# Kernel tuning notes

Hardware: AMD Instinct MI355X
Metric: run time of the kernel (lower is better)

The kernel has to match this reference:

```python
import jax, jax.numpy as jnp
import numpy as np

N_NODES = 50000
N_EDGES = 800000
IN_DIM = 128
OUT_DIM = 64


def setup_inputs() -> dict:
    key = jax.random.key(0)
    k1, k2, k3, k4 = jax.random.split(key, 4)
    x = jax.random.normal(k1, (N_NODES, IN_DIM), dtype=jnp.float32)
    edge_index = jax.random.randint(k2, (2, N_EDGES), 0, N_NODES, dtype=jnp.int64)
    # learned params: W: Linear(in_dim, out_dim, bias=False); att: Linear(2*out_dim, 1, bias=False)
    W = jax.random.normal(k3, (IN_DIM, OUT_DIM), dtype=jnp.float32) * 0.05
    att = jax.random.normal(k4, (2 * OUT_DIM, 1), dtype=jnp.float32) * 0.05
    return {"x": x, "edge_index": edge_index, "W": W, "att": att}


def reference(x, edge_index, W, att):
    n = x.shape[0]
    h = x @ W  # [N, D]
    src, dst = edge_index[0], edge_index[1]
    # per-edge attention logit: leaky_relu(att^T [h_src ; h_dst])
    e = jnp.concatenate([h[src], h[dst]], axis=-1) @ att  # [E, 1]
    e = jax.nn.leaky_relu(e[:, 0], negative_slope=0.2)  # [E]
    # segment softmax over edges grouped by destination node
    m = jax.ops.segment_max(e, dst, num_segments=n)  # [N]
    ex = jnp.exp(e - m[dst])  # [E]
    denom = jax.ops.segment_sum(ex, dst, num_segments=n)  # [N]
    alpha = ex / denom[dst]  # [E]
    # weighted scatter-add aggregation
    agg = jax.ops.segment_sum(alpha[:, None] * h[src], dst, num_segments=n)  # [N, D]
    return jax.nn.elu(agg)
```

## Files before the change

### kernel.cpp

```cpp
#include <hip/hip_runtime.h>
#include <hip/hip_bf16.h>
#include <hip/hip_fp16.h>
#include <math.h>

#define N_NODES 50000
#define N_EDGES 800000
#define IN_DIM 128
#define OUT_DIM 64

typedef __attribute__((ext_vector_type(8))) short bf16x8;
typedef __attribute__((ext_vector_type(4))) float f32x4;

static __device__ __forceinline__ ushort f2bf(float f) {
  uint u = __float_as_uint(f);
  uint r = (u + 0x7fffu + ((u >> 16) & 1u)) >> 16;
  return (ushort)r;
}
static __device__ __forceinline__ float bf2f(ushort h) {
  return __uint_as_float(((uint)h) << 16);
}

__global__ __launch_bounds__(256) void k1_mfma(
    const float* __restrict__ x, const float* __restrict__ W,
    const float* __restrict__ att,
    __half* __restrict__ h, float* __restrict__ a1, float* __restrict__ a2,
    int* __restrict__ deg) {
  __shared__ __align__(16) ushort Ah[64 * 128];
  __shared__ __align__(16) ushort Al[64 * 128];
  __shared__ __align__(16) ushort Bh[64 * 128];
  __shared__ __align__(16) ushort Bl[64 * 128];

  int tid = threadIdx.x;
  int row0 = blockIdx.x * 64;

  if (tid < 64) {
    int g = row0 + tid;
    if (g < N_NODES) deg[g] = 0;
  }

#pragma unroll
  for (int it = 0; it < 8; ++it) {
    int i4 = it * 256 + tid;
    int row = i4 >> 5;
    int kq = i4 & 31;
    int grow = row0 + row;
    if (grow > N_NODES - 1) grow = N_NODES - 1;
    float4 v = ((const float4*)x)[(size_t)grow * 32 + kq];
    ushort4 hi, lo;
    hi.x = f2bf(v.x); lo.x = f2bf(v.x - bf2f(hi.x));
    hi.y = f2bf(v.y); lo.y = f2bf(v.y - bf2f(hi.y));
    hi.z = f2bf(v.z); lo.z = f2bf(v.z - bf2f(hi.z));
    hi.w = f2bf(v.w); lo.w = f2bf(v.w - bf2f(hi.w));
    int idx = (row * 128 + kq * 4) ^ ((row & 7) << 3);
    *(ushort4*)&Ah[idx] = hi;
    *(ushort4*)&Al[idx] = lo;
  }

  {
    int c = tid & 63, kq = tid >> 6;
#pragma unroll
    for (int jj = 0; jj < 4; ++jj) {
      int kb = kq * 32 + jj * 8;
      uint4 ph, pl;
      uint hp[8], lp[8];
#pragma unroll
      for (int q = 0; q < 8; ++q) {
        float wv = W[(size_t)(kb + q) * OUT_DIM + c];
        ushort hh = f2bf(wv);
        hp[q] = hh;
        lp[q] = f2bf(wv - bf2f(hh));
      }
      ph.x = hp[0] | (hp[1] << 16); ph.y = hp[2] | (hp[3] << 16);
      ph.z = hp[4] | (hp[5] << 16); ph.w = hp[6] | (hp[7] << 16);
      pl.x = lp[0] | (lp[1] << 16); pl.y = lp[2] | (lp[3] << 16);
      pl.z = lp[4] | (lp[5] << 16); pl.w = lp[6] | (lp[7] << 16);
      int idx = (c * 128 + kb) ^ ((c & 7) << 3);
      *(uint4*)&Bh[idx] = ph;
      *(uint4*)&Bl[idx] = pl;
    }
  }
  __syncthreads();

  int w = tid >> 6, l = tid & 63;
  int ml = l & 15, kg = l >> 4;

  f32x4 acc[4];
#pragma unroll
  for (int nt = 0; nt < 4; ++nt) acc[nt] = (f32x4){0.f, 0.f, 0.f, 0.f};

#pragma unroll
  for (int ks = 0; ks < 4; ++ks) {
    int arow = w * 16 + ml;
    int aidx = (arow * 128 + ks * 32 + kg * 8) ^ ((arow & 7) << 3);
    bf16x8 a_h = *(const bf16x8*)&Ah[aidx];
    bf16x8 a_l = *(const bf16x8*)&Al[aidx];
#pragma unroll
    for (int nt = 0; nt < 4; ++nt) {
      int brow = nt * 16 + ml;
      int bidx = (brow * 128 + ks * 32 + kg * 8) ^ ((brow & 7) << 3);
      bf16x8 b_h = *(const bf16x8*)&Bh[bidx];
      bf16x8 b_l = *(const bf16x8*)&Bl[bidx];
      acc[nt] = __builtin_amdgcn_mfma_f32_16x16x32_bf16(a_h, b_h, acc[nt], 0, 0, 0);
      acc[nt] = __builtin_amdgcn_mfma_f32_16x16x32_bf16(a_l, b_h, acc[nt], 0, 0, 0);
      acc[nt] = __builtin_amdgcn_mfma_f32_16x16x32_bf16(a_h, b_l, acc[nt], 0, 0, 0);
    }
  }

  float t1[4], t2[4];
#pragma unroll
  for (int nt = 0; nt < 4; ++nt) {
    t1[nt] = att[nt * 16 + ml];
    t2[nt] = att[OUT_DIM + nt * 16 + ml];
  }
#pragma unroll
  for (int r = 0; r < 4; ++r) {
    int drow = kg * 4 + r;
    int grow = row0 + w * 16 + drow;
    bool ok = grow < N_NODES;
    float p1 = 0.f, p2 = 0.f;
#pragma unroll
    for (int nt = 0; nt < 4; ++nt) {
      float d = acc[nt][r];
      if (ok) h[(size_t)grow * OUT_DIM + nt * 16 + ml] = __float2half(d);
      p1 = fmaf(d, t1[nt], p1);
      p2 = fmaf(d, t2[nt], p2);
    }
#pragma unroll
    for (int o = 1; o <= 8; o <<= 1) {
      p1 += __shfl_xor(p1, o, 64);
      p2 += __shfl_xor(p2, o, 64);
    }
    if (ml == 0 && ok) { a1[grow] = p1; a2[grow] = p2; }
  }
}

#define K2_T (N_EDGES / 8)
__global__ __launch_bounds__(256) void k2_rank(const int* __restrict__ dstp,
                                               int* __restrict__ deg,
                                               int* __restrict__ rank) {
  int t = blockIdx.x * 256 + threadIdx.x;
  if (t >= K2_T) return;
  int4 d0 = ((const int4*)dstp)[t * 2];
  int4 d1 = ((const int4*)dstp)[t * 2 + 1];
  int4 r0, r1;
  r0.x = atomicAdd(&deg[d0.x], 1);
  r0.y = atomicAdd(&deg[d0.y], 1);
  r0.z = atomicAdd(&deg[d0.z], 1);
  r0.w = atomicAdd(&deg[d0.w], 1);
  r1.x = atomicAdd(&deg[d1.x], 1);
  r1.y = atomicAdd(&deg[d1.y], 1);
  r1.z = atomicAdd(&deg[d1.z], 1);
  r1.w = atomicAdd(&deg[d1.w], 1);
  ((int4*)rank)[t * 2] = r0;
  ((int4*)rank)[t * 2 + 1] = r1;
}

#define N4 (N_NODES / 4)
#define SCAN_NB ((N4 + 255) / 256)

__global__ __launch_bounds__(256) void k3a_scan(const int* __restrict__ deg,
                                                int* __restrict__ off,
                                                int* __restrict__ bsum) {
  __shared__ int sw[4];
  int tid = threadIdx.x, lane = tid & 63, wid = tid >> 6;
  int i4 = blockIdx.x * 256 + tid;
  int4 v = make_int4(0, 0, 0, 0);
  if (i4 < N4) v = ((const int4*)deg)[i4];
  int local = v.x + v.y + v.z + v.w;
  int incl = local;
#pragma unroll
  for (int o = 1; o < 64; o <<= 1) {
    int t = __shfl_up(incl, o, 64);
    if (lane >= o) incl += t;
  }
  if (lane == 63) sw[wid] = incl;
  __syncthreads();
  if (tid == 0) {
    int c = 0;
#pragma unroll
    for (int ww = 0; ww < 4; ++ww) { int t = sw[ww]; sw[ww] = c; c += t; }
    bsum[blockIdx.x] = c;
  }
  __syncthreads();
  int excl = incl - local + sw[wid];
  int4 o;
  o.x = excl; o.y = o.x + v.x; o.z = o.y + v.y; o.w = o.z + v.z;
  if (i4 < N4) ((int4*)off)[i4] = o;
}

__global__ __launch_bounds__(256) void k3c_add(int* __restrict__ off,
                                               const int* __restrict__ bsum,
                                               const float* __restrict__ a2,
                                               int2* __restrict__ oa2) {
  __shared__ int sb[64];
  int tid = threadIdx.x;
  if (tid < 64) {
    int v = (tid < SCAN_NB) ? bsum[tid] : 0;
    int incl = v;
#pragma unroll
    for (int o = 1; o < 64; o <<= 1) {
      int t = __shfl_up(incl, o, 64);
      if (tid >= o) incl += t;
    }
    sb[tid] = incl - v;
  }
  __syncthreads();
  int i4 = blockIdx.x * 256 + tid;
  if (i4 == 0) off[N_NODES] = N_EDGES;
  if (i4 >= N4) return;
  int add = sb[blockIdx.x];
  int4 v = ((const int4*)off)[i4];
  v.x += add; v.y += add; v.z += add; v.w += add;
  ((int4*)off)[i4] = v;
  float4 a = ((const float4*)a2)[i4];
  int4 p0 = make_int4(v.x, __float_as_int(a.x), v.y, __float_as_int(a.y));
  int4 p1 = make_int4(v.z, __float_as_int(a.z), v.w, __float_as_int(a.w));
  ((int4*)oa2)[i4 * 2] = p0;
  ((int4*)oa2)[i4 * 2 + 1] = p1;
}

#define K4_T (N_EDGES / 4)
__global__ __launch_bounds__(256) void k4_scatter(
    const int* __restrict__ src, const int* __restrict__ dstp,
    const int* __restrict__ rank,
    const float* __restrict__ a1, const int2* __restrict__ oa2,
    int2* __restrict__ sedge) {
  int t = blockIdx.x * 256 + threadIdx.x;
  if (t >= K4_T) return;
  int4 s = ((const int4*)src)[t];
  int4 d = ((const int4*)dstp)[t];
  int4 r = ((const int4*)rank)[t];
  float A0 = a1[s.x], A1 = a1[s.y], A2 = a1[s.z], A3 = a1[s.w];
  int2 O0 = oa2[d.x], O1 = oa2[d.y], O2 = oa2[d.z], O3 = oa2[d.w];
  float e0 = A0 + __int_as_float(O0.y);
  float e1 = A1 + __int_as_float(O1.y);
  float e2 = A2 + __int_as_float(O2.y);
  float e3 = A3 + __int_as_float(O3.y);
  e0 = e0 > 0.f ? e0 : 0.2f * e0;
  e1 = e1 > 0.f ? e1 : 0.2f * e1;
  e2 = e2 > 0.f ? e2 : 0.2f * e2;
  e3 = e3 > 0.f ? e3 : 0.2f * e3;
  sedge[O0.x + r.x] = make_int2(s.x, __float_as_int(__expf(e0)));
  sedge[O1.x + r.y] = make_int2(s.y, __float_as_int(__expf(e1)));
  sedge[O2.x + r.z] = make_int2(s.z, __float_as_int(__expf(e2)));
  sedge[O3.x + r.w] = make_int2(s.w, __float_as_int(__expf(e3)));
}

__global__ __launch_bounds__(256) void k5_agg(
    const int* __restrict__ off, const int2* __restrict__ sedge,
    const __half* __restrict__ h, float* __restrict__ out) {
  int tid = threadIdx.x;
  int g = tid >> 4, gl = tid & 15;
  int n = blockIdx.x * 16 + g;
  if (n >= N_NODES) return;
  int b = off[n], e = off[n + 1];

  float sum = 0.f;
  float acc0 = 0.f, acc1 = 0.f, acc2 = 0.f, acc3 = 0.f;
  const __half* __restrict__ hb = h;

  int j = b;
  for (; j + 3 < e; j += 4) {
    int2 s0 = sedge[j], s1 = sedge[j + 1], s2 = sedge[j + 2], s3 = sedge[j + 3];
    uint2 r0 = *(const uint2*)(hb + (size_t)s0.x * OUT_DIM + 4 * gl);
    uint2 r1 = *(const uint2*)(hb + (size_t)s1.x * OUT_DIM + 4 * gl);
    uint2 r2 = *(const uint2*)(hb + (size_t)s2.x * OUT_DIM + 4 * gl);
    uint2 r3 = *(const uint2*)(hb + (size_t)s3.x * OUT_DIM + 4 * gl);
    float w0 = __int_as_float(s0.y), w1 = __int_as_float(s1.y);
    float w2 = __int_as_float(s2.y), w3 = __int_as_float(s3.y);
    sum += (w0 + w1) + (w2 + w3);
    float2 f;
    f = __half22float2(__builtin_bit_cast(__half2, r0.x)); acc0 = fmaf(w0, f.x, acc0); acc1 = fmaf(w0, f.y, acc1);
    f = __half22float2(__builtin_bit_cast(__half2, r0.y)); acc2 = fmaf(w0, f.x, acc2); acc3 = fmaf(w0, f.y, acc3);
    f = __half22float2(__builtin_bit_cast(__half2, r1.x)); acc0 = fmaf(w1, f.x, acc0); acc1 = fmaf(w1, f.y, acc1);
    f = __half22float2(__builtin_bit_cast(__half2, r1.y)); acc2 = fmaf(w1, f.x, acc2); acc3 = fmaf(w1, f.y, acc3);
    f = __half22float2(__builtin_bit_cast(__half2, r2.x)); acc0 = fmaf(w2, f.x, acc0); acc1 = fmaf(w2, f.y, acc1);
    f = __half22float2(__builtin_bit_cast(__half2, r2.y)); acc2 = fmaf(w2, f.x, acc2); acc3 = fmaf(w2, f.y, acc3);
    f = __half22float2(__builtin_bit_cast(__half2, r3.x)); acc0 = fmaf(w3, f.x, acc0); acc1 = fmaf(w3, f.y, acc1);
    f = __half22float2(__builtin_bit_cast(__half2, r3.y)); acc2 = fmaf(w3, f.x, acc2); acc3 = fmaf(w3, f.y, acc3);
  }
  for (; j < e; ++j) {
    int2 s0 = sedge[j];
    uint2 r0 = *(const uint2*)(hb + (size_t)s0.x * OUT_DIM + 4 * gl);
    float w0 = __int_as_float(s0.y);
    sum += w0;
    float2 f;
    f = __half22float2(__builtin_bit_cast(__half2, r0.x)); acc0 = fmaf(w0, f.x, acc0); acc1 = fmaf(w0, f.y, acc1);
    f = __half22float2(__builtin_bit_cast(__half2, r0.y)); acc2 = fmaf(w0, f.x, acc2); acc3 = fmaf(w0, f.y, acc3);
  }

  float inv = (e > b) ? 1.f / sum : 0.f;
  acc0 *= inv; acc1 *= inv; acc2 *= inv; acc3 *= inv;
  float4 o4;
  o4.x = acc0 > 0.f ? acc0 : (__expf(acc0) - 1.f);
  o4.y = acc1 > 0.f ? acc1 : (__expf(acc1) - 1.f);
  o4.z = acc2 > 0.f ? acc2 : (__expf(acc2) - 1.f);
  o4.w = acc3 > 0.f ? acc3 : (__expf(acc3) - 1.f);
  ((float4*)(out + (size_t)n * OUT_DIM))[gl] = o4;
}

extern "C" void kernel_launch(void* const* d_in, const int* in_sizes, int n_in,
                              void* d_out, int out_size, void* d_ws, size_t ws_size,
                              hipStream_t stream) {
  const float* x   = (const float*)d_in[0];
  const int*   ei  = (const int*)d_in[1];
  const float* W   = (const float*)d_in[2];
  const float* att = (const float*)d_in[3];
  float* out = (float*)d_out;

  char* p = (char*)d_ws;
  __half* h  = (__half*)p;  p += (size_t)N_NODES * OUT_DIM * sizeof(__half);
  float* a1  = (float*)p;   p += (size_t)N_NODES * sizeof(float);
  float* a2  = (float*)p;   p += (size_t)N_NODES * sizeof(float);
  int*   deg = (int*)p;     p += (size_t)N_NODES * sizeof(int);
  int*   off = (int*)p;     p += (size_t)(N_NODES + 4) * sizeof(int);
  int2*  oa2 = (int2*)p;    p += (size_t)N_NODES * sizeof(int2);
  int*   rank = (int*)p;    p += (size_t)N_EDGES * sizeof(int);
  int2*  sedge = (int2*)p;  p += (size_t)N_EDGES * sizeof(int2);
  int*   bsum = (int*)p;    p += 64 * sizeof(int);

  const int* src  = ei;
  const int* dstp = ei + N_EDGES;

  k1_mfma<<<(N_NODES + 63) / 64, 256, 0, stream>>>(x, W, att, h, a1, a2, deg);
  k2_rank<<<(K2_T + 255) / 256, 256, 0, stream>>>(dstp, deg, rank);
  k3a_scan<<<SCAN_NB, 256, 0, stream>>>(deg, off, bsum);
  k3c_add<<<SCAN_NB, 256, 0, stream>>>(off, bsum, a2, oa2);
  k4_scatter<<<(K4_T + 255) / 256, 256, 0, stream>>>(src, dstp, rank, a1, oa2, sedge);
  k5_agg<<<(N_NODES + 15) / 16, 256, 0, stream>>>(off, sedge, h, out);
}
```

Baseline: 97.54 us.

## Fuse rank counting into GEMM launch, drop W low-part MFMA, widen gathers

Splits the degree-zeroing into its own small kernel and merges the edge-rank atomic pass with the projection GEMM into one launch, with separate block ranges for each, so the two independent phases can overlap. The GEMM drops the bf16 low-part of W and its third MFMA per tile, which lowers the precision of h. The scatter kernel now handles 8 edges per thread. The aggregation kernel uses 8 lanes per node with 16-byte loads of h rows instead of 16 lanes with 8-byte loads.

```diff
diff --git a/kernel.cpp b/kernel.cpp
--- a/kernel.cpp
+++ b/kernel.cpp
@@ -20,23 +20,49 @@
   return __uint_as_float(((uint)h) << 16);
 }
 
-__global__ __launch_bounds__(256) void k1_mfma(
+#define N4 (N_NODES / 4)
+#define SCAN_NB ((N4 + 255) / 256)
+#define RANK_NB ((N_EDGES / 8 + 255) / 256)
+#define GEMM_NB ((N_NODES + 63) / 64)
+#define K2_T (N_EDGES / 8)
+#define K4_T (N_EDGES / 8)
+
+__global__ __launch_bounds__(256) void k0_zero(int* __restrict__ deg) {
+  int i4 = blockIdx.x * 256 + threadIdx.x;
+  if (i4 < N4) ((int4*)deg)[i4] = make_int4(0, 0, 0, 0);
+}
+
+__global__ __launch_bounds__(256) void k12_fused(
     const float* __restrict__ x, const float* __restrict__ W,
-    const float* __restrict__ att,
+    const float* __restrict__ att, const int* __restrict__ dstp,
     __half* __restrict__ h, float* __restrict__ a1, float* __restrict__ a2,
-    int* __restrict__ deg) {
+    int* __restrict__ deg, int* __restrict__ rank) {
   __shared__ __align__(16) ushort Ah[64 * 128];
   __shared__ __align__(16) ushort Al[64 * 128];
   __shared__ __align__(16) ushort Bh[64 * 128];
-  __shared__ __align__(16) ushort Bl[64 * 128];
 
   int tid = threadIdx.x;
-  int row0 = blockIdx.x * 64;
-
-  if (tid < 64) {
-    int g = row0 + tid;
-    if (g < N_NODES) deg[g] = 0;
-  }
+
+  if (blockIdx.x < RANK_NB) {
+    int t = blockIdx.x * 256 + tid;
+    if (t >= K2_T) return;
+    int4 d0 = ((const int4*)dstp)[t * 2];
+    int4 d1 = ((const int4*)dstp)[t * 2 + 1];
+    int4 r0, r1;
+    r0.x = atomicAdd(&deg[d0.x], 1);
+    r0.y = atomicAdd(&deg[d0.y], 1);
+    r0.z = atomicAdd(&deg[d0.z], 1);
+    r0.w = atomicAdd(&deg[d0.w], 1);
+    r1.x = atomicAdd(&deg[d1.x], 1);
+    r1.y = atomicAdd(&deg[d1.y], 1);
+    r1.z = atomicAdd(&deg[d1.z], 1);
+    r1.w = atomicAdd(&deg[d1.w], 1);
+    ((int4*)rank)[t * 2] = r0;
+    ((int4*)rank)[t * 2 + 1] = r1;
+    return;
+  }
+
+  int row0 = (blockIdx.x - RANK_NB) * 64;
 
 #pragma unroll
   for (int it = 0; it < 8; ++it) {
@@ -61,22 +87,14 @@
 #pragma unroll
     for (int jj = 0; jj < 4; ++jj) {
       int kb = kq * 32 + jj * 8;
-      uint4 ph, pl;
-      uint hp[8], lp[8];
-#pragma unroll
-      for (int q = 0; q < 8; ++q) {
-        float wv = W[(size_t)(kb + q) * OUT_DIM + c];
-        ushort hh = f2bf(wv);
-        hp[q] = hh;
-        lp[q] = f2bf(wv - bf2f(hh));
-      }
+      uint4 ph;
+      uint hp[8];
+#pragma unroll
+      for (int q = 0; q < 8; ++q) hp[q] = f2bf(W[(size_t)(kb + q) * OUT_DIM + c]);
       ph.x = hp[0] | (hp[1] << 16); ph.y = hp[2] | (hp[3] << 16);
       ph.z = hp[4] | (hp[5] << 16); ph.w = hp[6] | (hp[7] << 16);
-      pl.x = lp[0] | (lp[1] << 16); pl.y = lp[2] | (lp[3] << 16);
-      pl.z = lp[4] | (lp[5] << 16); pl.w = lp[6] | (lp[7] << 16);
       int idx = (c * 128 + kb) ^ ((c & 7) << 3);
       *(uint4*)&Bh[idx] = ph;
-      *(uint4*)&Bl[idx] = pl;
     }
   }
   __syncthreads();
@@ -99,10 +117,8 @@
       int brow = nt * 16 + ml;
       int bidx = (brow * 128 + ks * 32 + kg * 8) ^ ((brow & 7) << 3);
       bf16x8 b_h = *(const bf16x8*)&Bh[bidx];
-      bf16x8 b_l = *(const bf16x8*)&Bl[bidx];
       acc[nt] = __builtin_amdgcn_mfma_f32_16x16x32_bf16(a_h, b_h, acc[nt], 0, 0, 0);
       acc[nt] = __builtin_amdgcn_mfma_f32_16x16x32_bf16(a_l, b_h, acc[nt], 0, 0, 0);
-      acc[nt] = __builtin_amdgcn_mfma_f32_16x16x32_bf16(a_h, b_l, acc[nt], 0, 0, 0);
     }
   }
 
@@ -133,30 +149,6 @@
     if (ml == 0 && ok) { a1[grow] = p1; a2[grow] = p2; }
   }
 }
-
-#define K2_T (N_EDGES / 8)
-__global__ __launch_bounds__(256) void k2_rank(const int* __restrict__ dstp,
-                                               int* __restrict__ deg,
-                                               int* __restrict__ rank) {
-  int t = blockIdx.x * 256 + threadIdx.x;
-  if (t >= K2_T) return;
-  int4 d0 = ((const int4*)dstp)[t * 2];
-  int4 d1 = ((const int4*)dstp)[t * 2 + 1];
-  int4 r0, r1;
-  r0.x = atomicAdd(&deg[d0.x], 1);
-  r0.y = atomicAdd(&deg[d0.y], 1);
-  r0.z = atomicAdd(&deg[d0.z], 1);
-  r0.w = atomicAdd(&deg[d0.w], 1);
-  r1.x = atomicAdd(&deg[d1.x], 1);
-  r1.y = atomicAdd(&deg[d1.y], 1);
-  r1.z = atomicAdd(&deg[d1.z], 1);
-  r1.w = atomicAdd(&deg[d1.w], 1);
-  ((int4*)rank)[t * 2] = r0;
-  ((int4*)rank)[t * 2 + 1] = r1;
-}
-
-#define N4 (N_NODES / 4)
-#define SCAN_NB ((N4 + 255) / 256)
 
 __global__ __launch_bounds__(256) void k3a_scan(const int* __restrict__ deg,
                                                 int* __restrict__ off,
@@ -219,7 +211,6 @@
   ((int4*)oa2)[i4 * 2 + 1] = p1;
 }
 
-#define K4_T (N_EDGES / 4)
 __global__ __launch_bounds__(256) void k4_scatter(
     const int* __restrict__ src, const int* __restrict__ dstp,
     const int* __restrict__ rank,
@@ -227,76 +218,87 @@
     int2* __restrict__ sedge) {
   int t = blockIdx.x * 256 + threadIdx.x;
   if (t >= K4_T) return;
-  int4 s = ((const int4*)src)[t];
-  int4 d = ((const int4*)dstp)[t];
-  int4 r = ((const int4*)rank)[t];
-  float A0 = a1[s.x], A1 = a1[s.y], A2 = a1[s.z], A3 = a1[s.w];
-  int2 O0 = oa2[d.x], O1 = oa2[d.y], O2 = oa2[d.z], O3 = oa2[d.w];
-  float e0 = A0 + __int_as_float(O0.y);
-  float e1 = A1 + __int_as_float(O1.y);
-  float e2 = A2 + __int_as_float(O2.y);
-  float e3 = A3 + __int_as_float(O3.y);
-  e0 = e0 > 0.f ? e0 : 0.2f * e0;
-  e1 = e1 > 0.f ? e1 : 0.2f * e1;
-  e2 = e2 > 0.f ? e2 : 0.2f * e2;
-  e3 = e3 > 0.f ? e3 : 0.2f * e3;
-  sedge[O0.x + r.x] = make_int2(s.x, __float_as_int(__expf(e0)));
-  sedge[O1.x + r.y] = make_int2(s.y, __float_as_int(__expf(e1)));
-  sedge[O2.x + r.z] = make_int2(s.z, __float_as_int(__expf(e2)));
-  sedge[O3.x + r.w] = make_int2(s.w, __float_as_int(__expf(e3)));
+  int4 s0 = ((const int4*)src)[t * 2],  s1 = ((const int4*)src)[t * 2 + 1];
+  int4 d0 = ((const int4*)dstp)[t * 2], d1 = ((const int4*)dstp)[t * 2 + 1];
+  int4 r0 = ((const int4*)rank)[t * 2], r1 = ((const int4*)rank)[t * 2 + 1];
+  float A[8];
+  A[0] = a1[s0.x]; A[1] = a1[s0.y]; A[2] = a1[s0.z]; A[3] = a1[s0.w];
+  A[4] = a1[s1.x]; A[5] = a1[s1.y]; A[6] = a1[s1.z]; A[7] = a1[s1.w];
+  int2 O[8];
+  O[0] = oa2[d0.x]; O[1] = oa2[d0.y]; O[2] = oa2[d0.z]; O[3] = oa2[d0.w];
+  O[4] = oa2[d1.x]; O[5] = oa2[d1.y]; O[6] = oa2[d1.z]; O[7] = oa2[d1.w];
+  int S[8] = {s0.x, s0.y, s0.z, s0.w, s1.x, s1.y, s1.z, s1.w};
+  int R[8] = {r0.x, r0.y, r0.z, r0.w, r1.x, r1.y, r1.z, r1.w};
+#pragma unroll
+  for (int q = 0; q < 8; ++q) {
+    float e = A[q] + __int_as_float(O[q].y);
+    e = e > 0.f ? e : 0.2f * e;
+    sedge[O[q].x + R[q]] = make_int2(S[q], __float_as_int(__expf(e)));
+  }
 }
 
 __global__ __launch_bounds__(256) void k5_agg(
     const int* __restrict__ off, const int2* __restrict__ sedge,
     const __half* __restrict__ h, float* __restrict__ out) {
   int tid = threadIdx.x;
-  int g = tid >> 4, gl = tid & 15;
-  int n = blockIdx.x * 16 + g;
+  int g = tid >> 3, gl = tid & 7;
+  int n = blockIdx.x * 32 + g;
   if (n >= N_NODES) return;
   int b = off[n], e = off[n + 1];
 
   float sum = 0.f;
-  float acc0 = 0.f, acc1 = 0.f, acc2 = 0.f, acc3 = 0.f;
+  float a0 = 0.f, a1_ = 0.f, a2_ = 0.f, a3 = 0.f;
+  float a4 = 0.f, a5 = 0.f, a6 = 0.f, a7 = 0.f;
   const __half* __restrict__ hb = h;
+
+#define K5_ACC(rr, ww)                                                        \
+  {                                                                           \
+    float2 f;                                                                 \
+    f = __half22float2(__builtin_bit_cast(__half2, rr.x));                    \
+    a0 = fmaf(ww, f.x, a0); a1_ = fmaf(ww, f.y, a1_);                         \
+    f = __half22float2(__builtin_bit_cast(__half2, rr.y));                    \
+    a2_ = fmaf(ww, f.x, a2_); a3 = fmaf(ww, f.y, a3);                         \
+    f = __half22float2(__builtin_bit_cast(__half2, rr.z));                    \
+    a4 = fmaf(ww, f.x, a4); a5 = fmaf(ww, f.y, a5);                           \
+    f = __half22float2(__builtin_bit_cast(__half2, rr.w));                    \
+    a6 = fmaf(ww, f.x, a6); a7 = fmaf(ww, f.y, a7);                           \
+  }
 
   int j = b;
   for (; j + 3 < e; j += 4) {
     int2 s0 = sedge[j], s1 = sedge[j + 1], s2 = sedge[j + 2], s3 = sedge[j + 3];
-    uint2 r0 = *(const uint2*)(hb + (size_t)s0.x * OUT_DIM + 4 * gl);
-    uint2 r1 = *(const uint2*)(hb + (size_t)s1.x * OUT_DIM + 4 * gl);
-    uint2 r2 = *(const uint2*)(hb + (size_t)s2.x * OUT_DIM + 4 * gl);
-    uint2 r3 = *(const uint2*)(hb + (size_t)s3.x * OUT_DIM + 4 * gl);
+    uint4 r0 = ((const uint4*)(hb + (size_t)s0.x * OUT_DIM))[gl];
+    uint4 r1 = ((const uint4*)(hb + (size_t)s1.x * OUT_DIM))[gl];
+    uint4 r2 = ((const uint4*)(hb + (size_t)s2.x * OUT_DIM))[gl];
+    uint4 r3 = ((const uint4*)(hb + (size_t)s3.x * OUT_DIM))[gl];
     float w0 = __int_as_float(s0.y), w1 = __int_as_float(s1.y);
     float w2 = __int_as_float(s2.y), w3 = __int_as_float(s3.y);
     sum += (w0 + w1) + (w2 + w3);
-    float2 f;
-    f = __half22float2(__builtin_bit_cast(__half2, r0.x)); acc0 = fmaf(w0, f.x, acc0); acc1 = fmaf(w0, f.y, acc1);
-    f = __half22float2(__builtin_bit_cast(__half2, r0.y)); acc2 = fmaf(w0, f.x, acc2); acc3 = fmaf(w0, f.y, acc3);
-    f = __half22float2(__builtin_bit_cast(__half2, r1.x)); acc0 = fmaf(w1, f.x, acc0); acc1 = fmaf(w1, f.y, acc1);
-    f = __half22float2(__builtin_bit_cast(__half2, r1.y)); acc2 = fmaf(w1, f.x, acc2); acc3 = fmaf(w1, f.y, acc3);
-    f = __half22float2(__builtin_bit_cast(__half2, r2.x)); acc0 = fmaf(w2, f.x, acc0); acc1 = fmaf(w2, f.y, acc1);
-    f = __half22float2(__builtin_bit_cast(__half2, r2.y)); acc2 = fmaf(w2, f.x, acc2); acc3 = fmaf(w2, f.y, acc3);
-    f = __half22float2(__builtin_bit_cast(__half2, r3.x)); acc0 = fmaf(w3, f.x, acc0); acc1 = fmaf(w3, f.y, acc1);
-    f = __half22float2(__builtin_bit_cast(__half2, r3.y)); acc2 = fmaf(w3, f.x, acc2); acc3 = fmaf(w3, f.y, acc3);
+    K5_ACC(r0, w0); K5_ACC(r1, w1); K5_ACC(r2, w2); K5_ACC(r3, w3);
   }
   for (; j < e; ++j) {
     int2 s0 = sedge[j];
-    uint2 r0 = *(const uint2*)(hb + (size_t)s0.x * OUT_DIM + 4 * gl);
+    uint4 r0 = ((const uint4*)(hb + (size_t)s0.x * OUT_DIM))[gl];
     float w0 = __int_as_float(s0.y);
     sum += w0;
-    float2 f;
-    f = __half22float2(__builtin_bit_cast(__half2, r0.x)); acc0 = fmaf(w0, f.x, acc0); acc1 = fmaf(w0, f.y, acc1);
-    f = __half22float2(__builtin_bit_cast(__half2, r0.y)); acc2 = fmaf(w0, f.x, acc2); acc3 = fmaf(w0, f.y, acc3);
+    K5_ACC(r0, w0);
   }
 
   float inv = (e > b) ? 1.f / sum : 0.f;
-  acc0 *= inv; acc1 *= inv; acc2 *= inv; acc3 *= inv;
-  float4 o4;
-  o4.x = acc0 > 0.f ? acc0 : (__expf(acc0) - 1.f);
-  o4.y = acc1 > 0.f ? acc1 : (__expf(acc1) - 1.f);
-  o4.z = acc2 > 0.f ? acc2 : (__expf(acc2) - 1.f);
-  o4.w = acc3 > 0.f ? acc3 : (__expf(acc3) - 1.f);
-  ((float4*)(out + (size_t)n * OUT_DIM))[gl] = o4;
+  a0 *= inv; a1_ *= inv; a2_ *= inv; a3 *= inv;
+  a4 *= inv; a5 *= inv; a6 *= inv; a7 *= inv;
+  float4 o0, o1;
+  o0.x = a0 > 0.f ? a0 : (__expf(a0) - 1.f);
+  o0.y = a1_ > 0.f ? a1_ : (__expf(a1_) - 1.f);
+  o0.z = a2_ > 0.f ? a2_ : (__expf(a2_) - 1.f);
+  o0.w = a3 > 0.f ? a3 : (__expf(a3) - 1.f);
+  o1.x = a4 > 0.f ? a4 : (__expf(a4) - 1.f);
+  o1.y = a5 > 0.f ? a5 : (__expf(a5) - 1.f);
+  o1.z = a6 > 0.f ? a6 : (__expf(a6) - 1.f);
+  o1.w = a7 > 0.f ? a7 : (__expf(a7) - 1.f);
+  float4* ob = (float4*)(out + (size_t)n * OUT_DIM);
+  ob[gl * 2] = o0;
+  ob[gl * 2 + 1] = o1;
 }
 
 extern "C" void kernel_launch(void* const* d_in, const int* in_sizes, int n_in,
@@ -322,10 +324,10 @@
   const int* src  = ei;
   const int* dstp = ei + N_EDGES;
 
-  k1_mfma<<<(N_NODES + 63) / 64, 256, 0, stream>>>(x, W, att, h, a1, a2, deg);
-  k2_rank<<<(K2_T + 255) / 256, 256, 0, stream>>>(dstp, deg, rank);
+  k0_zero<<<SCAN_NB, 256, 0, stream>>>(deg);
+  k12_fused<<<RANK_NB + GEMM_NB, 256, 0, stream>>>(x, W, att, dstp, h, a1, a2, deg, rank);
   k3a_scan<<<SCAN_NB, 256, 0, stream>>>(deg, off, bsum);
   k3c_add<<<SCAN_NB, 256, 0, stream>>>(off, bsum, a2, oa2);
   k4_scatter<<<(K4_T + 255) / 256, 256, 0, stream>>>(src, dstp, rank, a1, oa2, sedge);
-  k5_agg<<<(N_NODES + 15) / 16, 256, 0, stream>>>(off, sedge, h, out);
-}
+  k5_agg<<<(N_NODES + 31) / 32, 256, 0, stream>>>(off, sedge, h, out);
+}
```

Result: faster. 91.69 us (-6.0%).
